# Kernel optimization log

Hardware: AMD Instinct MI355X
Metric: run time of the kernel (lower is better)

The kernel has to match this reference:

```python
import jax, jax.numpy as jnp
import numpy as np

NUM_HEADS = 8
NSCALE = 2  # len(sr_ratio) + 1 with sr_ratio=[2.0]


def setup_inputs() -> dict:
    key = jax.random.key(0)
    ks = jax.random.split(key, 12)
    B, Nq, Np, C, n_up, N_all = 16, 1024, 1024, 512, 2048, 4096
    s = C ** -0.5  # keep attention logits in a sane range
    return {
        "query": jax.random.normal(ks[0], (Nq, B, C), jnp.float32),
        "key": jax.random.normal(ks[1], (Np, B, C), jnp.float32),
        "key_pos": jax.random.uniform(ks[2], (B, Np, 3), jnp.float32),
        "xyz_all": jax.random.uniform(ks[3], (B, N_all, 3), jnp.float32),
        "xyz_upsample": jax.random.uniform(ks[4], (B, n_up, 3), jnp.float32),
        "Wq": jax.random.normal(ks[5], (C, C), jnp.float32) * s,
        "Wkv1": jax.random.normal(ks[6], (C, C), jnp.float32) * s,
        "Wkv2": jax.random.normal(ks[7], (C, C), jnp.float32) * s,
        "fp_w": jax.random.normal(ks[8], (C, C), jnp.float32) * s,
        "fp_b": jnp.zeros((C,), jnp.float32),
        "proj_w": jax.random.normal(ks[9], (C, C), jnp.float32) * s,
        "proj_b": jnp.zeros((C,), jnp.float32),
    }


def _fp_upsample(xyz_up, key_pos, key_feats, fp_w, fp_b):
    """PointnetFPModuleUpSample: 3-NN inverse-distance feature interpolation
    from Np known points (key_pos) onto n_up target points, followed by a
    pointwise MLP (1x1 conv, BN folded) + ReLU.
    key_feats: (Np, B, C) -> returns (B, n_up, C)."""
    d2 = jnp.sum((xyz_up[:, :, None, :] - key_pos[:, None, :, :]) ** 2, axis=-1)  # (B, n, Np)
    negd, idx = jax.lax.top_k(-d2, 3)  # 3 nearest neighbors, (B, n, 3)
    w = 1.0 / (-negd + 1e-8)
    w = w / jnp.sum(w, axis=-1, keepdims=True)
    feats = jnp.transpose(key_feats, (1, 0, 2))  # (B, Np, C)
    g = jnp.take_along_axis(feats[:, None, :, :], idx[..., None], axis=2)  # (B, n, 3, C)
    interp = jnp.sum(g * w[..., None], axis=2)  # (B, n, C)
    return jax.nn.relu(interp @ fp_w.T + fp_b)


def reference(query, key, key_pos, xyz_all, xyz_upsample,
              Wq, Wkv1, Wkv2, fp_w, fp_b, proj_w, proj_b):
    Np, B, C = key.shape
    Nq = query.shape[0]
    H = NUM_HEADS
    nh = H // NSCALE  # heads per scale group
    hd = C // H
    scale = hd ** -0.5

    # NOTE: torch reshapes (N,B,C) -> (B,N,...) WITHOUT permuting first; we
    # replicate the identical row-major reshape for bit-faithful structure.
    q = (query @ Wq.T).reshape(B, Nq, H, hd).transpose(0, 2, 1, 3)  # (B,H,Nq,hd)

    def attend(qs, kv):
        k, v = kv[0], kv[1]
        a = jax.nn.softmax(jnp.einsum('bhqd,bhkd->bhqk', qs, k) * scale, axis=-1)
        o = jnp.einsum('bhqk,bhkd->bhqd', a, v)
        return o.transpose(0, 2, 1, 3).reshape(B, Nq, nh * hd)

    # scale 1: full-resolution keys
    kv1 = (key @ Wkv1.T).reshape(B, -1, 2, nh, hd).transpose(2, 0, 3, 1, 4)
    x1 = attend(q[:, :nh], kv1)

    # scale 2: FP-upsampled keys (sr_ratio=2.0 -> 2*base_np points)
    key2 = _fp_upsample(xyz_upsample, key_pos, key, fp_w, fp_b)  # (B, n, C)
    key2_nbc = key2.transpose(1, 0, 2)  # (n, B, C), matches permute(2,0,1) of (B,C,n)
    kv2 = (key2_nbc @ Wkv2.T).reshape(B, -1, 2, nh, hd).transpose(2, 0, 3, 1, 4)
    x2 = attend(q[:, nh:], kv2)

    x = jnp.concatenate([x1, x2], axis=-1) @ proj_w.T + proj_b  # (B, Nq, C)
    return x.transpose(1, 0, 2)  # (Nq, B, C)
```

## Files before the change

kernel.cpp:

```cpp
#include <hip/hip_runtime.h>
#include <cstdint>
#include <cstddef>

#define CD   512
#define BDIM 16
#define NQ   1024
#define NP   1024
#define NUP  2048

typedef unsigned short u16;
typedef short short8 __attribute__((ext_vector_type(8)));
typedef float f32x4  __attribute__((ext_vector_type(4)));
typedef uint32_t u32x4 __attribute__((ext_vector_type(4)));

#define GLOAD16(g, l) __builtin_amdgcn_global_load_lds( \
    (const __attribute__((address_space(1))) void*)(g), \
    (__attribute__((address_space(3))) void*)(l), 16, 0, 0)

__device__ __forceinline__ u16 rne_bf16(float x) {
  uint32_t u = __float_as_uint(x);
  return (u16)((u + 0x7fffu + ((u >> 16) & 1u)) >> 16);
}
__device__ __forceinline__ float bf2f(u16 v) {
  return __uint_as_float(((uint32_t)v) << 16);
}

__global__ __launch_bounds__(256) void prep_kernel(
    const float* __restrict__ query, u16* __restrict__ Qa,
    const float* __restrict__ key, u16* __restrict__ Ka,
    const float* __restrict__ Wq, const float* __restrict__ Wkv1,
    const float* __restrict__ projw, const float* __restrict__ fpw,
    const float* __restrict__ wkv2, u16* __restrict__ Wq2,
    u16* __restrict__ Wkv12, u16* __restrict__ proj2,
    u16* __restrict__ fpwb, u16* __restrict__ wkv2b,
    const float* __restrict__ key_pos, const float* __restrict__ xyz_up,
    int* __restrict__ idx_out, float* __restrict__ w_out)
{
  const int bx = blockIdx.x;
  const int tid = threadIdx.x;
  if (bx < 8832) {
    const float* in; u16* out; float scl = 1.0f; long u;
    if (bx < 8192) {
      in = (bx < 4096) ? query : key;
      out = (bx < 4096) ? Qa : Ka;
      u = (long)(bx & 4095) * 256 + tid;
    } else {
      const int job = (bx - 8192) >> 7;
      in  = (job == 0) ? Wq  : (job == 1) ? Wkv1  : (job == 2) ? projw : (job == 3) ? fpw  : wkv2;
      out = (job == 0) ? Wq2 : (job == 1) ? Wkv12 : (job == 2) ? proj2 : (job == 3) ? fpwb : wkv2b;
      if (job == 0) scl = 0.18033688011112042f;
      u = (long)((bx - 8192) & 127) * 256 + tid;
    }
    const float* ip = in + u * 8;
    float v[8];
    *(float4*)&v[0] = *(const float4*)ip;
    *(float4*)&v[4] = *(const float4*)(ip + 4);
    short8 o;
#pragma unroll
    for (int i = 0; i < 8; ++i) o[i] = (short)rne_bf16(v[i] * scl);
    *(short8*)(out + u * 8) = o;
    return;
  }
  __shared__ __align__(16) float4 kp4[NP];
  const int kb = bx - 8832;
  const int b = kb >> 7;
  const int n0 = (kb & 127) * 16;
  const float* kpb = key_pos + (long)b * NP * 3;
#pragma unroll
  for (int s = 0; s < 4; ++s) {
    const int t = s * 256 + tid;
    kp4[t] = make_float4(kpb[t * 3], kpb[t * 3 + 1], kpb[t * 3 + 2], 0.0f);
  }
  __syncthreads();
  const int sc = tid & 15, pt = tid >> 4;
  const int n = n0 + pt;
  const float ux = xyz_up[(b * NUP + n) * 3 + 0];
  const float uy = xyz_up[(b * NUP + n) * 3 + 1];
  const float uz = xyz_up[(b * NUP + n) * 3 + 2];
  float e0 = 3.4e38f, e1 = 3.4e38f, e2 = 3.4e38f;
  int j0 = 0, j1 = 0, j2 = 0;
  for (int it = 0; it < 64; ++it) {
    const int j = it * 16 + sc;
    const float4 kv = kp4[j];
    const float dx = ux - kv.x, dy = uy - kv.y, dz = uz - kv.z;
    const float dd = dx * dx + dy * dy + dz * dz;
    if (dd < e2) {
      if (dd < e1) {
        e2 = e1; j2 = j1;
        if (dd < e0) { e1 = e0; j1 = j0; e0 = dd; j0 = j; }
        else         { e1 = dd; j1 = j; }
      } else { e2 = dd; j2 = j; }
    }
  }
#pragma unroll
  for (int ms = 1; ms <= 8; ms <<= 1) {
    const float pd0 = __shfl_xor(e0, ms), pd1 = __shfl_xor(e1, ms), pd2 = __shfl_xor(e2, ms);
    const int   pi0 = __shfl_xor(j0, ms), pi1 = __shfl_xor(j1, ms), pi2 = __shfl_xor(j2, ms);
    float cd[3] = {pd0, pd1, pd2};
    int   ci[3] = {pi0, pi1, pi2};
#pragma unroll
    for (int t = 0; t < 3; ++t) {
      const float dd = cd[t]; const int jj = ci[t];
      if (dd < e2 || (dd == e2 && jj < j2)) {
        if (dd < e1 || (dd == e1 && jj < j1)) {
          e2 = e1; j2 = j1;
          if (dd < e0 || (dd == e0 && jj < j0)) { e1 = e0; j1 = j0; e0 = dd; j0 = jj; }
          else                                  { e1 = dd; j1 = jj; }
        } else { e2 = dd; j2 = jj; }
      }
    }
  }
  if (sc == 0) {
    const float w0 = 1.0f / (e0 + 1e-8f);
    const float w1 = 1.0f / (e1 + 1e-8f);
    const float w2 = 1.0f / (e2 + 1e-8f);
    const float inv = 1.0f / ((w0 + w1) + w2);
    const long r = (long)b * NUP + n;
    idx_out[r * 3 + 0] = j0; idx_out[r * 3 + 1] = j1; idx_out[r * 3 + 2] = j2;
    w_out[r * 3 + 0] = w0 * inv; w_out[r * 3 + 1] = w1 * inv; w_out[r * 3 + 2] = w2 * inv;
  }
}

template<int AMODE, int OMODE, int KE, int NKT>
__device__ __forceinline__ void gemm_body64(
    u16* __restrict__ As, u16* __restrict__ Ws,
    const u16* __restrict__ A, const u16* __restrict__ W,
    const float* __restrict__ bias, void* __restrict__ outv,
    u16* __restrict__ Vt, const int m0, const int n0)
{
  const int tid = threadIdx.x;
  const int lane = tid & 63, wv = tid >> 6;
  const int rch = tid & 7;

  f32x4 acc[4][4];
#pragma unroll
  for (int mi = 0; mi < 4; ++mi)
#pragma unroll
    for (int ni = 0; ni < 4; ++ni)
#pragma unroll
      for (int r = 0; r < 4; ++r) acc[mi][ni][r] = 0.0f;

  const long rowb = (long)KE * 2;
  const char* gA[4]; const char* gW[4];
#pragma unroll
  for (int s = 0; s < 4; ++s) {
    const int row = s * 32 + (tid >> 3);
    const int gm = m0 + row;
    const long arow = (AMODE == 0) ? (long)gm : (long)(gm & 15) * 2048 + (gm >> 4);
    const int kb0 = (rch ^ (row & 7)) << 4;
    gA[s] = (const char*)A + arow * rowb + kb0;
    gW[s] = (const char*)W + (long)(n0 + row) * rowb + kb0;
  }
  const int wr = (wv >> 1) * 64, wc = (wv & 1) * 64;
  const int g = lane >> 4, cl = lane & 15;

  for (int kt = 0; kt < KE / 64; ++kt) {
#pragma unroll
    for (int s = 0; s < 4; ++s) {
      GLOAD16(gA[s], (char*)As + (s * 256 + tid) * 16);
      GLOAD16(gW[s], (char*)Ws + (s * 256 + tid) * 16);
      gA[s] += 128; gW[s] += 128;
    }
    __syncthreads();
#pragma unroll
    for (int kb = 0; kb < 2; ++kb) {
      short8 af[4], bf[4];
#pragma unroll
      for (int i = 0; i < 4; ++i) {
        const int ra = wr + i * 16 + cl;
        af[i] = *(const short8*)((const char*)As + ra * 128
                 + ((kb * 64 + g * 16) ^ ((ra & 7) << 4)));
        const int rb = wc + i * 16 + cl;
        bf[i] = *(const short8*)((const char*)Ws + rb * 128
                 + ((kb * 64 + g * 16) ^ ((rb & 7) << 4)));
      }
#pragma unroll
      for (int mi = 0; mi < 4; ++mi)
#pragma unroll
        for (int ni = 0; ni < 4; ++ni)
          acc[mi][ni] = __builtin_amdgcn_mfma_f32_16x16x32_bf16(af[mi], bf[ni], acc[mi][ni], 0, 0, 0);
    }
    __syncthreads();
  }

  if constexpr (OMODE == 3) {
    u16* T = As;
#pragma unroll
    for (int ni = 0; ni < 4; ++ni) {
      const int n = wc + ni * 16 + cl;
      const int swz = (n & 15) << 4;
      const int rb2 = n * 256;
#pragma unroll
      for (int mi = 0; mi < 4; ++mi) {
        uint32_t lo, hi;
        asm("v_cvt_pk_bf16_f32 %0, %1, %2" : "=v"(lo) : "v"(acc[mi][ni][0]), "v"(acc[mi][ni][1]));
        asm("v_cvt_pk_bf16_f32 %0, %1, %2" : "=v"(hi) : "v"(acc[mi][ni][2]), "v"(acc[mi][ni][3]));
        const int m2 = 2 * (wr + mi * 16 + g * 4);
        uint2 pk; pk.x = lo; pk.y = hi;
        *(uint2*)((char*)T + rb2 + (m2 ^ swz)) = pk;
      }
    }
    __syncthreads();
    const int nl = tid >> 1, mh = tid & 1;
    const int v = (n0 - 256) + nl;
    const int hh = v >> 6, dd = v & 63;
    const int bq = m0 / NKT;
    const int p0 = (m0 & (NKT - 1)) + mh * 64;
    u16* dst = Vt + ((size_t)((bq * 4 + hh) * 64 + dd)) * NKT + p0;
    const int swz = (nl & 15) << 4;
#pragma unroll
    for (int j = 0; j < 8; ++j) {
      const int m2 = mh * 128 + j * 16;
      const short8 val = *(const short8*)((const char*)T + nl * 256 + (m2 ^ swz));
      *(short8*)(dst + j * 8) = val;
    }
    return;
  } else {
#pragma unroll
    for (int mi = 0; mi < 4; ++mi)
#pragma unroll
      for (int ni = 0; ni < 4; ++ni)
#pragma unroll
        for (int r = 0; r < 4; ++r) {
          const int gm = m0 + wr + mi * 16 + g * 4 + r;
          const int gn = n0 + wc + ni * 16 + cl;
          float vv = acc[mi][ni][r];
          if (OMODE == 0) {
            ((u16*)outv)[(long)gm * 512 + gn] = rne_bf16(vv);
          } else if (OMODE == 1) {
            vv = fmaxf(vv + bias[gn], 0.0f);
            ((u16*)outv)[(long)gm * 512 + gn] = rne_bf16(vv);
          } else {
            vv += bias[gn];
            ((float*)outv)[((long)(gm & 1023) * BDIM + (gm >> 10)) * 512 + gn] = vv;
          }
        }
  }
}

template<int AMODE, int OMODE, int KE>
__global__ __launch_bounds__(256) void gemm_one(
    const u16* __restrict__ A, const u16* __restrict__ W,
    const float* __restrict__ bias, void* __restrict__ outv)
{
  __shared__ __align__(16) u16 SH[16384];
  gemm_body64<AMODE, OMODE, KE, 1024>(SH, SH + 8192, A, W, bias, outv, nullptr,
                                      blockIdx.x * 128, blockIdx.y * 128);
}

__global__ __launch_bounds__(256) void qkv1_interp_kernel(
    const u16* __restrict__ Qa, const u16* __restrict__ Wq2, u16* __restrict__ Qb,
    const u16* __restrict__ Ka, const u16* __restrict__ Wkv12,
    u16* __restrict__ KV1, u16* __restrict__ Vt1,
    const int* __restrict__ idx, const float* __restrict__ w, u16* __restrict__ IN2)
{
  __shared__ __align__(16) u16 SH[16384];
  const int bid = blockIdx.x;
  if (bid < 512) {
    gemm_body64<0, 0, 512, 1024>(SH, SH + 8192, Qa, Wq2, nullptr, Qb, nullptr,
                                 (bid >> 2) * 128, (bid & 3) * 128);
  } else if (bid < 1024) {
    const int t = bid - 512;
    const int n0 = (t & 3) * 128;
    if (n0 >= 256)
      gemm_body64<0, 3, 512, 1024>(SH, SH + 8192, Ka, Wkv12, nullptr, KV1, Vt1,
                                   (t >> 2) * 128, n0);
    else
      gemm_body64<0, 0, 512, 1024>(SH, SH + 8192, Ka, Wkv12, nullptr, KV1, nullptr,
                                   (t >> 2) * 128, n0);
  } else {
    const int t = threadIdx.x;
    const long r = (long)(bid - 1024) * 4 + (t >> 6);
    const int j = t & 63;
    const int b = (int)(r >> 11);
    const int j0 = idx[r * 3 + 0], j1 = idx[r * 3 + 1], j2 = idx[r * 3 + 2];
    const float w0 = w[r * 3 + 0], w1 = w[r * 3 + 1], w2 = w[r * 3 + 2];
    const short8 a0 = *(const short8*)(Ka + ((long)j0 * BDIM + b) * CD + j * 8);
    const short8 a1 = *(const short8*)(Ka + ((long)j1 * BDIM + b) * CD + j * 8);
    const short8 a2 = *(const short8*)(Ka + ((long)j2 * BDIM + b) * CD + j * 8);
    short8 o;
#pragma unroll
    for (int i = 0; i < 8; ++i)
      o[i] = (short)rne_bf16(bf2f((u16)a0[i]) * w0 + bf2f((u16)a1[i]) * w1
                           + bf2f((u16)a2[i]) * w2);
    *(short8*)(IN2 + r * CD + j * 8) = o;
  }
}

__global__ __launch_bounds__(256) void kv2_kernel(
    const u16* __restrict__ KEY2, const u16* __restrict__ wkv2b,
    u16* __restrict__ KV2, u16* __restrict__ Vt2)
{
  __shared__ __align__(16) u16 SH[16384];
  const int t = blockIdx.x;
  const int n0 = (t & 3) * 128;
  if (n0 >= 256)
    gemm_body64<1, 3, 512, 2048>(SH, SH + 8192, KEY2, wkv2b, nullptr, KV2, Vt2,
                                 (t >> 2) * 128, n0);
  else
    gemm_body64<1, 0, 512, 2048>(SH, SH + 8192, KEY2, wkv2b, nullptr, KV2, nullptr,
                                 (t >> 2) * 128, n0);
}

__global__ __launch_bounds__(256) void gemm_proj64_kernel(
    const u16* __restrict__ A, const u16* __restrict__ W,
    const float* __restrict__ bias, float* __restrict__ out)
{
  __shared__ __align__(16) u16 As[64 * 32];
  __shared__ __align__(16) u16 Ws[128 * 32];
  const int tid = threadIdx.x;
  const int lane = tid & 63, wv = tid >> 6;
  const int m0 = blockIdx.x * 64, n0 = blockIdx.y * 128;

  f32x4 acc[2][4];
#pragma unroll
  for (int mi = 0; mi < 2; ++mi)
#pragma unroll
    for (int ni = 0; ni < 4; ++ni)
#pragma unroll
      for (int r = 0; r < 4; ++r) acc[mi][ni][r] = 0.0f;

  const int ar = tid >> 2, ac = tid & 3;
  const char* gA = (const char*)A + (long)(m0 + ar) * 1024 + ((ac ^ (ar & 3)) << 4);
  const char* gW[2];
#pragma unroll
  for (int s = 0; s < 2; ++s) {
    const int rw = s * 64 + ar;
    gW[s] = (const char*)W + (long)(n0 + rw) * 1024 + ((ac ^ (rw & 3)) << 4);
  }
  const int wr = (wv >> 1) * 32, wc = (wv & 1) * 64;
  const int g = lane >> 4, cl = lane & 15;
  const int gx = (g ^ (cl & 3)) << 4;

  for (int kt = 0; kt < 16; ++kt) {
    GLOAD16(gA, (char*)As + tid * 16); gA += 64;
#pragma unroll
    for (int s = 0; s < 2; ++s) {
      GLOAD16(gW[s], (char*)Ws + (s * 256 + tid) * 16); gW[s] += 64;
    }
    __syncthreads();
    short8 af[2], bf[4];
#pragma unroll
    for (int i = 0; i < 2; ++i)
      af[i] = *(const short8*)((const char*)As + (wr + i * 16 + cl) * 64 + gx);
#pragma unroll
    for (int j = 0; j < 4; ++j)
      bf[j] = *(const short8*)((const char*)Ws + (wc + j * 16 + cl) * 64 + gx);
#pragma unroll
    for (int mi = 0; mi < 2; ++mi)
#pragma unroll
      for (int ni = 0; ni < 4; ++ni)
        acc[mi][ni] = __builtin_amdgcn_mfma_f32_16x16x32_bf16(af[mi], bf[ni], acc[mi][ni], 0, 0, 0);
    __syncthreads();
  }

#pragma unroll
  for (int mi = 0; mi < 2; ++mi)
#pragma unroll
    for (int ni = 0; ni < 4; ++ni)
#pragma unroll
      for (int r = 0; r < 4; ++r) {
        const int gm = m0 + wr + mi * 16 + g * 4 + r;
        const int gn = n0 + wc + ni * 16 + cl;
        out[((long)(gm & 1023) * BDIM + (gm >> 10)) * 512 + gn] = acc[mi][ni][r] + bias[gn];
      }
}

template<int NK>
__device__ __forceinline__ void attn_body(
    u16* __restrict__ Ks, u16* __restrict__ Vs,
    const u16* __restrict__ Q, const u16* __restrict__ KV,
    const u16* __restrict__ Vt, u16* __restrict__ X,
    const int h, const int sc, const int qt, const int b)
{
  const int tid = threadIdx.x;
  const int lane = tid & 63, wv = tid >> 6;
  const int g = lane >> 4, cl = lane & 15;

  const u16* qptr = Q + ((size_t)(b * 1024 + qt * 64 + wv * 16 + cl)) * 512
                      + (sc * 4 + h) * 64 + g * 8;
  const short8 qf0 = *(const short8*)qptr;
  const short8 qf1 = *(const short8*)(qptr + 32);

  f32x4 acc[4];
#pragma unroll
  for (int dj = 0; dj < 4; ++dj)
#pragma unroll
    for (int r = 0; r < 4; ++r) acc[dj][r] = 0.0f;
  float l = 0.0f;

  const char* kB = (const char*)(KV + (size_t)b * NK * 512 + h * 64);
  const char* vB = (const char*)(Vt + (size_t)((b * 4 + h) * 64) * NK);
  uint32_t koffL[4], voffL[4];
#pragma unroll
  for (int s = 0; s < 4; ++s) {
    const int c = s * 256 + tid;
    { const int rr = c >> 3, ch = c & 7;
      const int sig = (rr & 3) | ((rr >> 1) & 4);
      koffL[s] = rr * 1024 + ((ch ^ sig) << 4); }
    { const int rr = c >> 4, ch = c & 15;
      voffL[s] = rr * (NK * 2) + ((ch ^ (rr & 7)) << 4); }
  }

  int koffb[2][2];
#pragma unroll
  for (int half = 0; half < 2; ++half) {
    const int rest = ((cl & 12) << 1) + half * 4 + (cl & 3);
    const int swz = ((rest & 3) << 4) | ((rest & 8) << 3);
#pragma unroll
    for (int dh = 0; dh < 2; ++dh)
      koffb[half][dh] = rest * 128 + ((dh * 64 + g * 16) ^ swz);
  }
  int voffx[4][2];
#pragma unroll
  for (int dj = 0; dj < 4; ++dj) {
    const int vrow = dj * 16 + cl;
    const int base = vrow * 256 + ((g * 16) ^ ((vrow & 7) << 4));
    voffx[dj][0] = base; voffx[dj][1] = base ^ 64;
  }
  const int srcb = (lane & 48) | (g << 2);

  constexpr int NT = NK / 128;
#define ISSUE_K(kt_) { const char* kT_ = kB + (size_t)(kt_) * 131072; \
  _Pragma("unroll") for (int s_ = 0; s_ < 4; ++s_) \
    GLOAD16(kT_ + koffL[s_], (char*)Ks + s_ * 4096 + tid * 16); }
#define ISSUE_V(kt_) { const char* vT_ = vB + (size_t)(kt_) * 256; \
  _Pragma("unroll") for (int s_ = 0; s_ < 4; ++s_) \
    GLOAD16(vT_ + voffL[s_], (char*)Vs + s_ * 4096 + tid * 16); }

  asm volatile("s_waitcnt vmcnt(0)" ::: "memory");
  ISSUE_K(0);
  ISSUE_V(0);

  for (int kt = 0; kt < NT; ++kt) {
    asm volatile("s_waitcnt vmcnt(4)" ::: "memory");
    __builtin_amdgcn_s_barrier();
    __builtin_amdgcn_sched_barrier(0);

    f32x4 sv[8];
#pragma unroll
    for (int f = 0; f < 8; ++f)
#pragma unroll
      for (int r = 0; r < 4; ++r) sv[f][r] = 0.0f;
    __builtin_amdgcn_s_setprio(1);
#pragma unroll
    for (int ks = 0; ks < 4; ++ks)
#pragma unroll
      for (int half = 0; half < 2; ++half) {
        const int f = ks * 2 + half;
        const short8 ak0 = *(const short8*)((const char*)Ks + ks * 4096 + koffb[half][0]);
        const short8 ak1 = *(const short8*)((const char*)Ks + ks * 4096 + koffb[half][1]);
        sv[f] = __builtin_amdgcn_mfma_f32_16x16x32_bf16(ak0, qf0, sv[f], 0, 0, 0);
        sv[f] = __builtin_amdgcn_mfma_f32_16x16x32_bf16(ak1, qf1, sv[f], 0, 0, 0);
      }
    __builtin_amdgcn_s_setprio(0);

    asm volatile("s_waitcnt lgkmcnt(0)" ::: "memory");
    __builtin_amdgcn_s_barrier();
    __builtin_amdgcn_sched_barrier(0);
    if (kt + 1 < NT) { ISSUE_K(kt + 1); }

    float rs = 0.0f;
#pragma unroll
    for (int f = 0; f < 8; ++f)
#pragma unroll
      for (int r = 0; r < 4; ++r) {
        sv[f][r] = __builtin_amdgcn_exp2f(sv[f][r]);
        rs += sv[f][r];
      }
    rs += __shfl_xor(rs, 16);
    rs += __shfl_xor(rs, 32);
    l += rs;

    u32x4 pw[4];
#pragma unroll
    for (int ks = 0; ks < 4; ++ks) {
      asm("v_cvt_pk_bf16_f32 %0, %1, %2" : "=v"(pw[ks][0]) : "v"(sv[2*ks][0]),   "v"(sv[2*ks][1]));
      asm("v_cvt_pk_bf16_f32 %0, %1, %2" : "=v"(pw[ks][1]) : "v"(sv[2*ks][2]),   "v"(sv[2*ks][3]));
      asm("v_cvt_pk_bf16_f32 %0, %1, %2" : "=v"(pw[ks][2]) : "v"(sv[2*ks+1][0]), "v"(sv[2*ks+1][1]));
      asm("v_cvt_pk_bf16_f32 %0, %1, %2" : "=v"(pw[ks][3]) : "v"(sv[2*ks+1][2]), "v"(sv[2*ks+1][3]));
    }

    if (kt + 1 < NT) { asm volatile("s_waitcnt vmcnt(4)" ::: "memory"); }
    else             { asm volatile("s_waitcnt vmcnt(0)" ::: "memory"); }
    __builtin_amdgcn_s_barrier();
    __builtin_amdgcn_sched_barrier(0);

    __builtin_amdgcn_s_setprio(1);
#pragma unroll
    for (int ks = 0; ks < 4; ++ks) {
      const short8 pa = __builtin_bit_cast(short8, pw[ks]);
#pragma unroll
      for (int dj = 0; dj < 4; ++dj) {
        const short8 bv = *(const short8*)((const char*)Vs +
                          ((ks >> 1) * 128 + voffx[dj][ks & 1]));
        acc[dj] = __builtin_amdgcn_mfma_f32_16x16x32_bf16(pa, bv, acc[dj], 0, 0, 0);
      }
    }
    __builtin_amdgcn_s_setprio(0);

    asm volatile("s_waitcnt lgkmcnt(0)" ::: "memory");
    __builtin_amdgcn_s_barrier();
    __builtin_amdgcn_sched_barrier(0);
    if (kt + 1 < NT) { ISSUE_V(kt + 1); }
  }
#undef ISSUE_K
#undef ISSUE_V

  const float inv = 1.0f / l;
  float invr[4];
#pragma unroll
  for (int r = 0; r < 4; ++r) invr[r] = __shfl(inv, srcb | r);
#pragma unroll
  for (int dj = 0; dj < 4; ++dj)
#pragma unroll
    for (int r = 0; r < 4; ++r) {
      const long gq = b * 1024 + qt * 64 + wv * 16 + g * 4 + r;
      X[gq * 512 + sc * 256 + h * 64 + dj * 16 + cl] = rne_bf16(acc[dj][r] * invr[r]);
    }
}

__global__ __launch_bounds__(256, 4) void attn_fused_kernel(
    const u16* __restrict__ Q,
    const u16* __restrict__ KV1, const u16* __restrict__ KV2,
    const u16* __restrict__ Vt1, const u16* __restrict__ Vt2,
    u16* __restrict__ X)
{
  __shared__ __align__(16) u16 Ks[128 * 64];
  __shared__ __align__(16) u16 Vs[64 * 128];
  const int d = blockIdx.x + (blockIdx.y << 4) + (blockIdx.z << 8);
  const int qt = (d >> 3) & 15;
  const int grp = (d & 7) + ((d >> 7) << 3);
  const int b = grp & 15, z = grp >> 4;
  if (z < 4) attn_body<1024>(Ks, Vs, Q, KV1, Vt1, X, z, 0, qt, b);
  else       attn_body<2048>(Ks, Vs, Q, KV2, Vt2, X, z - 4, 1, qt, b);
}

extern "C" void kernel_launch(void* const* d_in, const int* in_sizes, int n_in,
                              void* d_out, int out_size, void* d_ws, size_t ws_size,
                              hipStream_t stream) {
  const float* query   = (const float*)d_in[0];
  const float* key     = (const float*)d_in[1];
  const float* key_pos = (const float*)d_in[2];
  const float* xyz_up  = (const float*)d_in[4];
  const float* Wq      = (const float*)d_in[5];
  const float* Wkv1    = (const float*)d_in[6];
  const float* Wkv2    = (const float*)d_in[7];
  const float* fp_w    = (const float*)d_in[8];
  const float* fp_b    = (const float*)d_in[9];
  const float* proj_w  = (const float*)d_in[10];
  const float* proj_b  = (const float*)d_in[11];

  char* ws = (char*)d_ws;
  const size_t MB = 1024 * 1024;
  u16*  Qa    = (u16*)(ws + 0);
  u16*  Ka    = (u16*)(ws + 16 * MB);
  u16*  Qb    = (u16*)(ws + 32 * MB);
  u16*  KV1   = (u16*)(ws + 48 * MB);
  u16*  IN2   = (u16*)(ws + 64 * MB);
  u16*  KEY2  = (u16*)(ws + 96 * MB);
  u16*  Vt1   = (u16*)(ws + 128 * MB);
  u16*  Vt2   = (u16*)(ws + 136 * MB);
  u16*  Wq2   = (u16*)(ws + 152 * MB);
  u16*  Wkv12 = (u16*)(ws + 152 * MB + 512 * 1024);
  u16*  proj2 = (u16*)(ws + 153 * MB);
  u16*  fpwb  = (u16*)(ws + 153 * MB + 512 * 1024);
  u16*  wkv2b = (u16*)(ws + 154 * MB);
  int*  idxb  = (int*)(ws + 155 * MB);
  float* wb   = (float*)(ws + 156 * MB);
  u16*  KV2   = IN2;
  u16*  X     = Qa;

  prep_kernel<<<dim3(10880), 256, 0, stream>>>(
      query, Qa, key, Ka, Wq, Wkv1, proj_w, fp_w, Wkv2,
      Wq2, Wkv12, proj2, fpwb, wkv2b, key_pos, xyz_up, idxb, wb);
  qkv1_interp_kernel<<<dim3(9216), 256, 0, stream>>>(
      Qa, Wq2, Qb, Ka, Wkv12, KV1, Vt1, idxb, wb, IN2);
  gemm_one<0, 1, 512><<<dim3(256, 4), 256, 0, stream>>>(IN2, fpwb, fp_b, KEY2);
  kv2_kernel<<<dim3(1024), 256, 0, stream>>>(KEY2, wkv2b, KV2, Vt2);
  attn_fused_kernel<<<dim3(16, 16, 8), 256, 0, stream>>>(Qb, KV1, KV2, Vt1, Vt2, X);
  gemm_proj64_kernel<<<dim3(256, 4), 256, 0, stream>>>(X, proj2, proj_b, (float*)d_out);
}
```

Baseline: 234.3 us.

## Co-schedule scale-1 attention with KV2 GEMM in a single launch

The fused attention kernel is split. Scale-1 attention blocks, which depend only on Q and KV1, now run in the same grid as the KV2 projection GEMM. A separate kernel then handles scale-2 attention after KV2 is ready. This overlaps independent work and fills the GPU better during the GEMM. The cost is a heterogeneous kernel with GEMM-sized shared memory and no occupancy hint for the attention blocks, plus tail imbalance between the two block types.

```diff
diff --git a/kernel.cpp b/kernel.cpp
--- a/kernel.cpp
+++ b/kernel.cpp
@@ -246,6 +246,160 @@
   __shared__ __align__(16) u16 SH[16384];
   gemm_body64<AMODE, OMODE, KE, 1024>(SH, SH + 8192, A, W, bias, outv, nullptr,
                                       blockIdx.x * 128, blockIdx.y * 128);
+}
+
+template<int NK>
+__device__ __forceinline__ void attn_body(
+    u16* __restrict__ Ks, u16* __restrict__ Vs,
+    const u16* __restrict__ Q, const u16* __restrict__ KV,
+    const u16* __restrict__ Vt, u16* __restrict__ X,
+    const int h, const int sc, const int qt, const int b)
+{
+  const int tid = threadIdx.x;
+  const int lane = tid & 63, wv = tid >> 6;
+  const int g = lane >> 4, cl = lane & 15;
+
+  const u16* qptr = Q + ((size_t)(b * 1024 + qt * 64 + wv * 16 + cl)) * 512
+                      + (sc * 4 + h) * 64 + g * 8;
+  const short8 qf0 = *(const short8*)qptr;
+  const short8 qf1 = *(const short8*)(qptr + 32);
+
+  f32x4 acc[4];
+#pragma unroll
+  for (int dj = 0; dj < 4; ++dj)
+#pragma unroll
+    for (int r = 0; r < 4; ++r) acc[dj][r] = 0.0f;
+  float l = 0.0f;
+
+  const char* kB = (const char*)(KV + (size_t)b * NK * 512 + h * 64);
+  const char* vB = (const char*)(Vt + (size_t)((b * 4 + h) * 64) * NK);
+  uint32_t koffL[4], voffL[4];
+#pragma unroll
+  for (int s = 0; s < 4; ++s) {
+    const int c = s * 256 + tid;
+    { const int rr = c >> 3, ch = c & 7;
+      const int sig = (rr & 3) | ((rr >> 1) & 4);
+      koffL[s] = rr * 1024 + ((ch ^ sig) << 4); }
+    { const int rr = c >> 4, ch = c & 15;
+      voffL[s] = rr * (NK * 2) + ((ch ^ (rr & 7)) << 4); }
+  }
+
+  int koffb[2][2];
+#pragma unroll
+  for (int half = 0; half < 2; ++half) {
+    const int rest = ((cl & 12) << 1) + half * 4 + (cl & 3);
+    const int swz = ((rest & 3) << 4) | ((rest & 8) << 3);
+#pragma unroll
+    for (int dh = 0; dh < 2; ++dh)
+      koffb[half][dh] = rest * 128 + ((dh * 64 + g * 16) ^ swz);
+  }
+  int voffx[4][2];
+#pragma unroll
+  for (int dj = 0; dj < 4; ++dj) {
+    const int vrow = dj * 16 + cl;
+    const int base = vrow * 256 + ((g * 16) ^ ((vrow & 7) << 4));
+    voffx[dj][0] = base; voffx[dj][1] = base ^ 64;
+  }
+  const int srcb = (lane & 48) | (g << 2);
+
+  constexpr int NT = NK / 128;
+#define ISSUE_K(kt_) { const char* kT_ = kB + (size_t)(kt_) * 131072; \
+  _Pragma("unroll") for (int s_ = 0; s_ < 4; ++s_) \
+    GLOAD16(kT_ + koffL[s_], (char*)Ks + s_ * 4096 + tid * 16); }
+#define ISSUE_V(kt_) { const char* vT_ = vB + (size_t)(kt_) * 256; \
+  _Pragma("unroll") for (int s_ = 0; s_ < 4; ++s_) \
+    GLOAD16(vT_ + voffL[s_], (char*)Vs + s_ * 4096 + tid * 16); }
+
+  asm volatile("s_waitcnt vmcnt(0)" ::: "memory");
+  ISSUE_K(0);
+  ISSUE_V(0);
+
+  for (int kt = 0; kt < NT; ++kt) {
+    asm volatile("s_waitcnt vmcnt(4)" ::: "memory");
+    __builtin_amdgcn_s_barrier();
+    __builtin_amdgcn_sched_barrier(0);
+
+    f32x4 sv[8];
+#pragma unroll
+    for (int f = 0; f < 8; ++f)
+#pragma unroll
+      for (int r = 0; r < 4; ++r) sv[f][r] = 0.0f;
+    __builtin_amdgcn_s_setprio(1);
+#pragma unroll
+    for (int ks = 0; ks < 4; ++ks)
+#pragma unroll
+      for (int half = 0; half < 2; ++half) {
+        const int f = ks * 2 + half;
+        const short8 ak0 = *(const short8*)((const char*)Ks + ks * 4096 + koffb[half][0]);
+        const short8 ak1 = *(const short8*)((const char*)Ks + ks * 4096 + koffb[half][1]);
+        sv[f] = __builtin_amdgcn_mfma_f32_16x16x32_bf16(ak0, qf0, sv[f], 0, 0, 0);
+        sv[f] = __builtin_amdgcn_mfma_f32_16x16x32_bf16(ak1, qf1, sv[f], 0, 0, 0);
+      }
+    __builtin_amdgcn_s_setprio(0);
+
+    asm volatile("s_waitcnt lgkmcnt(0)" ::: "memory");
+    __builtin_amdgcn_s_barrier();
+    __builtin_amdgcn_sched_barrier(0);
+    if (kt + 1 < NT) { ISSUE_K(kt + 1); }
+
+    float rs = 0.0f;
+#pragma unroll
+    for (int f = 0; f < 8; ++f)
+#pragma unroll
+      for (int r = 0; r < 4; ++r) {
+        sv[f][r] = __builtin_amdgcn_exp2f(sv[f][r]);
+        rs += sv[f][r];
+      }
+    rs += __shfl_xor(rs, 16);
+    rs += __shfl_xor(rs, 32);
+    l += rs;
+
+    u32x4 pw[4];
+#pragma unroll
+    for (int ks = 0; ks < 4; ++ks) {
+      asm("v_cvt_pk_bf16_f32 %0, %1, %2" : "=v"(pw[ks][0]) : "v"(sv[2*ks][0]),   "v"(sv[2*ks][1]));
+      asm("v_cvt_pk_bf16_f32 %0, %1, %2" : "=v"(pw[ks][1]) : "v"(sv[2*ks][2]),   "v"(sv[2*ks][3]));
+      asm("v_cvt_pk_bf16_f32 %0, %1, %2" : "=v"(pw[ks][2]) : "v"(sv[2*ks+1][0]), "v"(sv[2*ks+1][1]));
+      asm("v_cvt_pk_bf16_f32 %0, %1, %2" : "=v"(pw[ks][3]) : "v"(sv[2*ks+1][2]), "v"(sv[2*ks+1][3]));
+    }
+
+    if (kt + 1 < NT) { asm volatile("s_waitcnt vmcnt(4)" ::: "memory"); }
+    else             { asm volatile("s_waitcnt vmcnt(0)" ::: "memory"); }
+    __builtin_amdgcn_s_barrier();
+    __builtin_amdgcn_sched_barrier(0);
+
+    __builtin_amdgcn_s_setprio(1);
+#pragma unroll
+    for (int ks = 0; ks < 4; ++ks) {
+      const short8 pa = __builtin_bit_cast(short8, pw[ks]);
+#pragma unroll
+      for (int dj = 0; dj < 4; ++dj) {
+        const short8 bv = *(const short8*)((const char*)Vs +
+                          ((ks >> 1) * 128 + voffx[dj][ks & 1]));
+        acc[dj] = __builtin_amdgcn_mfma_f32_16x16x32_bf16(pa, bv, acc[dj], 0, 0, 0);
+      }
+    }
+    __builtin_amdgcn_s_setprio(0);
+
+    asm volatile("s_waitcnt lgkmcnt(0)" ::: "memory");
+    __builtin_amdgcn_s_barrier();
+    __builtin_amdgcn_sched_barrier(0);
+    if (kt + 1 < NT) { ISSUE_V(kt + 1); }
+  }
+#undef ISSUE_K
+#undef ISSUE_V
+
+  const float inv = 1.0f / l;
+  float invr[4];
+#pragma unroll
+  for (int r = 0; r < 4; ++r) invr[r] = __shfl(inv, srcb | r);
+#pragma unroll
+  for (int dj = 0; dj < 4; ++dj)
+#pragma unroll
+    for (int r = 0; r < 4; ++r) {
+      const long gq = b * 1024 + qt * 64 + wv * 16 + g * 4 + r;
+      X[gq * 512 + sc * 256 + h * 64 + dj * 16 + cl] = rne_bf16(acc[dj][r] * invr[r]);
+    }
 }
 
 __global__ __launch_bounds__(256) void qkv1_interp_kernel(
@@ -287,19 +441,42 @@
   }
 }
 
-__global__ __launch_bounds__(256) void kv2_kernel(
+__global__ __launch_bounds__(256) void kv2_attn1_kernel(
     const u16* __restrict__ KEY2, const u16* __restrict__ wkv2b,
-    u16* __restrict__ KV2, u16* __restrict__ Vt2)
+    u16* __restrict__ KV2, u16* __restrict__ Vt2,
+    const u16* __restrict__ Qb, const u16* __restrict__ KV1,
+    const u16* __restrict__ Vt1, u16* __restrict__ X)
 {
   __shared__ __align__(16) u16 SH[16384];
-  const int t = blockIdx.x;
-  const int n0 = (t & 3) * 128;
-  if (n0 >= 256)
-    gemm_body64<1, 3, 512, 2048>(SH, SH + 8192, KEY2, wkv2b, nullptr, KV2, Vt2,
-                                 (t >> 2) * 128, n0);
-  else
-    gemm_body64<1, 0, 512, 2048>(SH, SH + 8192, KEY2, wkv2b, nullptr, KV2, nullptr,
-                                 (t >> 2) * 128, n0);
+  const int bid = blockIdx.x;
+  if (bid < 1024) {
+    const int n0 = (bid & 3) * 128;
+    if (n0 >= 256)
+      gemm_body64<1, 3, 512, 2048>(SH, SH + 8192, KEY2, wkv2b, nullptr, KV2, Vt2,
+                                   (bid >> 2) * 128, n0);
+    else
+      gemm_body64<1, 0, 512, 2048>(SH, SH + 8192, KEY2, wkv2b, nullptr, KV2, nullptr,
+                                   (bid >> 2) * 128, n0);
+  } else {
+    const int d = bid - 1024;
+    const int qt = (d >> 3) & 15;
+    const int grp = (d & 7) + ((d >> 7) << 3);
+    const int b = grp & 15, h = grp >> 4;
+    attn_body<1024>(SH, SH + 8192, Qb, KV1, Vt1, X, h, 0, qt, b);
+  }
+}
+
+__global__ __launch_bounds__(256, 4) void attn_s2_kernel(
+    const u16* __restrict__ Q, const u16* __restrict__ KV2,
+    const u16* __restrict__ Vt2, u16* __restrict__ X)
+{
+  __shared__ __align__(16) u16 Ks[128 * 64];
+  __shared__ __align__(16) u16 Vs[64 * 128];
+  const int d = blockIdx.x + (blockIdx.y << 4) + (blockIdx.z << 8);
+  const int qt = (d >> 3) & 15;
+  const int grp = (d & 7) + ((d >> 7) << 3);
+  const int b = grp & 15, h = grp >> 4;
+  attn_body<2048>(Ks, Vs, Q, KV2, Vt2, X, h, 1, qt, b);
 }
 
 __global__ __launch_bounds__(256) void gemm_proj64_kernel(
@@ -364,176 +541,6 @@
         const int gn = n0 + wc + ni * 16 + cl;
         out[((long)(gm & 1023) * BDIM + (gm >> 10)) * 512 + gn] = acc[mi][ni][r] + bias[gn];
       }
-}
-
-template<int NK>
-__device__ __forceinline__ void attn_body(
-    u16* __restrict__ Ks, u16* __restrict__ Vs,
-    const u16* __restrict__ Q, const u16* __restrict__ KV,
-    const u16* __restrict__ Vt, u16* __restrict__ X,
-    const int h, const int sc, const int qt, const int b)
-{
-  const int tid = threadIdx.x;
-  const int lane = tid & 63, wv = tid >> 6;
-  const int g = lane >> 4, cl = lane & 15;
-
-  const u16* qptr = Q + ((size_t)(b * 1024 + qt * 64 + wv * 16 + cl)) * 512
-                      + (sc * 4 + h) * 64 + g * 8;
-  const short8 qf0 = *(const short8*)qptr;
-  const short8 qf1 = *(const short8*)(qptr + 32);
-
-  f32x4 acc[4];
-#pragma unroll
-  for (int dj = 0; dj < 4; ++dj)
-#pragma unroll
-    for (int r = 0; r < 4; ++r) acc[dj][r] = 0.0f;
-  float l = 0.0f;
-
-  const char* kB = (const char*)(KV + (size_t)b * NK * 512 + h * 64);
-  const char* vB = (const char*)(Vt + (size_t)((b * 4 + h) * 64) * NK);
-  uint32_t koffL[4], voffL[4];
-#pragma unroll
-  for (int s = 0; s < 4; ++s) {
-    const int c = s * 256 + tid;
-    { const int rr = c >> 3, ch = c & 7;
-      const int sig = (rr & 3) | ((rr >> 1) & 4);
-      koffL[s] = rr * 1024 + ((ch ^ sig) << 4); }
-    { const int rr = c >> 4, ch = c & 15;
-      voffL[s] = rr * (NK * 2) + ((ch ^ (rr & 7)) << 4); }
-  }
-
-  int koffb[2][2];
-#pragma unroll
-  for (int half = 0; half < 2; ++half) {
-    const int rest = ((cl & 12) << 1) + half * 4 + (cl & 3);
-    const int swz = ((rest & 3) << 4) | ((rest & 8) << 3);
-#pragma unroll
-    for (int dh = 0; dh < 2; ++dh)
-      koffb[half][dh] = rest * 128 + ((dh * 64 + g * 16) ^ swz);
-  }
-  int voffx[4][2];
-#pragma unroll
-  for (int dj = 0; dj < 4; ++dj) {
-    const int vrow = dj * 16 + cl;
-    const int base = vrow * 256 + ((g * 16) ^ ((vrow & 7) << 4));
-    voffx[dj][0] = base; voffx[dj][1] = base ^ 64;
-  }
-  const int srcb = (lane & 48) | (g << 2);
-
-  constexpr int NT = NK / 128;
-#define ISSUE_K(kt_) { const char* kT_ = kB + (size_t)(kt_) * 131072; \
-  _Pragma("unroll") for (int s_ = 0; s_ < 4; ++s_) \
-    GLOAD16(kT_ + koffL[s_], (char*)Ks + s_ * 4096 + tid * 16); }
-#define ISSUE_V(kt_) { const char* vT_ = vB + (size_t)(kt_) * 256; \
-  _Pragma("unroll") for (int s_ = 0; s_ < 4; ++s_) \
-    GLOAD16(vT_ + voffL[s_], (char*)Vs + s_ * 4096 + tid * 16); }
-
-  asm volatile("s_waitcnt vmcnt(0)" ::: "memory");
-  ISSUE_K(0);
-  ISSUE_V(0);
-
-  for (int kt = 0; kt < NT; ++kt) {
-    asm volatile("s_waitcnt vmcnt(4)" ::: "memory");
-    __builtin_amdgcn_s_barrier();
-    __builtin_amdgcn_sched_barrier(0);
-
-    f32x4 sv[8];
-#pragma unroll
-    for (int f = 0; f < 8; ++f)
-#pragma unroll
-      for (int r = 0; r < 4; ++r) sv[f][r] = 0.0f;
-    __builtin_amdgcn_s_setprio(1);
-#pragma unroll
-    for (int ks = 0; ks < 4; ++ks)
-#pragma unroll
-      for (int half = 0; half < 2; ++half) {
-        const int f = ks * 2 + half;
-        const short8 ak0 = *(const short8*)((const char*)Ks + ks * 4096 + koffb[half][0]);
-        const short8 ak1 = *(const short8*)((const char*)Ks + ks * 4096 + koffb[half][1]);
-        sv[f] = __builtin_amdgcn_mfma_f32_16x16x32_bf16(ak0, qf0, sv[f], 0, 0, 0);
-        sv[f] = __builtin_amdgcn_mfma_f32_16x16x32_bf16(ak1, qf1, sv[f], 0, 0, 0);
-      }
-    __builtin_amdgcn_s_setprio(0);
-
-    asm volatile("s_waitcnt lgkmcnt(0)" ::: "memory");
-    __builtin_amdgcn_s_barrier();
-    __builtin_amdgcn_sched_barrier(0);
-    if (kt + 1 < NT) { ISSUE_K(kt + 1); }
-
-    float rs = 0.0f;
-#pragma unroll
-    for (int f = 0; f < 8; ++f)
-#pragma unroll
-      for (int r = 0; r < 4; ++r) {
-        sv[f][r] = __builtin_amdgcn_exp2f(sv[f][r]);
-        rs += sv[f][r];
-      }
-    rs += __shfl_xor(rs, 16);
-    rs += __shfl_xor(rs, 32);
-    l += rs;
-
-    u32x4 pw[4];
-#pragma unroll
-    for (int ks = 0; ks < 4; ++ks) {
-      asm("v_cvt_pk_bf16_f32 %0, %1, %2" : "=v"(pw[ks][0]) : "v"(sv[2*ks][0]),   "v"(sv[2*ks][1]));
-      asm("v_cvt_pk_bf16_f32 %0, %1, %2" : "=v"(pw[ks][1]) : "v"(sv[2*ks][2]),   "v"(sv[2*ks][3]));
-      asm("v_cvt_pk_bf16_f32 %0, %1, %2" : "=v"(pw[ks][2]) : "v"(sv[2*ks+1][0]), "v"(sv[2*ks+1][1]));
-      asm("v_cvt_pk_bf16_f32 %0, %1, %2" : "=v"(pw[ks][3]) : "v"(sv[2*ks+1][2]), "v"(sv[2*ks+1][3]));
-    }
-
-    if (kt + 1 < NT) { asm volatile("s_waitcnt vmcnt(4)" ::: "memory"); }
-    else             { asm volatile("s_waitcnt vmcnt(0)" ::: "memory"); }
-    __builtin_amdgcn_s_barrier();
-    __builtin_amdgcn_sched_barrier(0);
-
-    __builtin_amdgcn_s_setprio(1);
-#pragma unroll
-    for (int ks = 0; ks < 4; ++ks) {
-      const short8 pa = __builtin_bit_cast(short8, pw[ks]);
-#pragma unroll
-      for (int dj = 0; dj < 4; ++dj) {
-        const short8 bv = *(const short8*)((const char*)Vs +
-                          ((ks >> 1) * 128 + voffx[dj][ks & 1]));
-        acc[dj] = __builtin_amdgcn_mfma_f32_16x16x32_bf16(pa, bv, acc[dj], 0, 0, 0);
-      }
-    }
-    __builtin_amdgcn_s_setprio(0);
-
-    asm volatile("s_waitcnt lgkmcnt(0)" ::: "memory");
-    __builtin_amdgcn_s_barrier();
-    __builtin_amdgcn_sched_barrier(0);
-    if (kt + 1 < NT) { ISSUE_V(kt + 1); }
-  }
-#undef ISSUE_K
-#undef ISSUE_V
-
-  const float inv = 1.0f / l;
-  float invr[4];
-#pragma unroll
-  for (int r = 0; r < 4; ++r) invr[r] = __shfl(inv, srcb | r);
-#pragma unroll
-  for (int dj = 0; dj < 4; ++dj)
-#pragma unroll
-    for (int r = 0; r < 4; ++r) {
-      const long gq = b * 1024 + qt * 64 + wv * 16 + g * 4 + r;
-      X[gq * 512 + sc * 256 + h * 64 + dj * 16 + cl] = rne_bf16(acc[dj][r] * invr[r]);
-    }
-}
-
-__global__ __launch_bounds__(256, 4) void attn_fused_kernel(
-    const u16* __restrict__ Q,
-    const u16* __restrict__ KV1, const u16* __restrict__ KV2,
-    const u16* __restrict__ Vt1, const u16* __restrict__ Vt2,
-    u16* __restrict__ X)
-{
-  __shared__ __align__(16) u16 Ks[128 * 64];
-  __shared__ __align__(16) u16 Vs[64 * 128];
-  const int d = blockIdx.x + (blockIdx.y << 4) + (blockIdx.z << 8);
-  const int qt = (d >> 3) & 15;
-  const int grp = (d & 7) + ((d >> 7) << 3);
-  const int b = grp & 15, z = grp >> 4;
-  if (z < 4) attn_body<1024>(Ks, Vs, Q, KV1, Vt1, X, z, 0, qt, b);
-  else       attn_body<2048>(Ks, Vs, Q, KV2, Vt2, X, z - 4, 1, qt, b);
 }
 
 extern "C" void kernel_launch(void* const* d_in, const int* in_sizes, int n_in,
@@ -577,7 +584,8 @@
   qkv1_interp_kernel<<<dim3(9216), 256, 0, stream>>>(
       Qa, Wq2, Qb, Ka, Wkv12, KV1, Vt1, idxb, wb, IN2);
   gemm_one<0, 1, 512><<<dim3(256, 4), 256, 0, stream>>>(IN2, fpwb, fp_b, KEY2);
-  kv2_kernel<<<dim3(1024), 256, 0, stream>>>(KEY2, wkv2b, KV2, Vt2);
-  attn_fused_kernel<<<dim3(16, 16, 8), 256, 0, stream>>>(Qb, KV1, KV2, Vt1, Vt2, X);
+  kv2_attn1_kernel<<<dim3(2048), 256, 0, stream>>>(
+      KEY2, wkv2b, KV2, Vt2, Qb, KV1, Vt1, X);
+  attn_s2_kernel<<<dim3(16, 16, 4), 256, 0, stream>>>(Qb, KV2, Vt2, X);
   gemm_proj64_kernel<<<dim3(256, 4), 256, 0, stream>>>(X, proj2, proj_b, (float*)d_out);
 }
```

Result: no change. 237.8 us (+1.5%).

## Switch attention to 32x32x16 MFMA with 128-query tiles and merged K/V loads

Applied to the files above, without the earlier changes.

Rewrites the fused attention body to use 32x32x16 bf16 MFMA instead of 16x16x32, so each wave handles 32 queries and each block 128. That halves the grid and doubles K/V reuse per LDS tile. K and V tiles are now loaded together, with a full vmcnt(0) wait, instead of being staged separately, and the LDS swizzles are redone for the new fragment layout. The softmax row sum no longer needs per-tile shuffles, but the merged loads lose the previous overlap of V loading with QK compute and fewer blocks run concurrently.

```diff
diff --git a/kernel.cpp b/kernel.cpp
--- a/kernel.cpp
+++ b/kernel.cpp
@@ -11,6 +11,7 @@
 typedef unsigned short u16;
 typedef short short8 __attribute__((ext_vector_type(8)));
 typedef float f32x4  __attribute__((ext_vector_type(4)));
+typedef float f32x16 __attribute__((ext_vector_type(16)));
 typedef uint32_t u32x4 __attribute__((ext_vector_type(4)));
 
 #define GLOAD16(g, l) __builtin_amdgcn_global_load_lds( \
@@ -367,7 +368,7 @@
 }
 
 template<int NK>
-__device__ __forceinline__ void attn_body(
+__device__ __forceinline__ void attn_body32(
     u16* __restrict__ Ks, u16* __restrict__ Vs,
     const u16* __restrict__ Q, const u16* __restrict__ KV,
     const u16* __restrict__ Vt, u16* __restrict__ X,
@@ -375,18 +376,17 @@
 {
   const int tid = threadIdx.x;
   const int lane = tid & 63, wv = tid >> 6;
-  const int g = lane >> 4, cl = lane & 15;
-
-  const u16* qptr = Q + ((size_t)(b * 1024 + qt * 64 + wv * 16 + cl)) * 512
-                      + (sc * 4 + h) * 64 + g * 8;
-  const short8 qf0 = *(const short8*)qptr;
-  const short8 qf1 = *(const short8*)(qptr + 32);
-
-  f32x4 acc[4];
-#pragma unroll
-  for (int dj = 0; dj < 4; ++dj)
-#pragma unroll
-    for (int r = 0; r < 4; ++r) acc[dj][r] = 0.0f;
+  const int hi = lane >> 5, ql = lane & 31;
+
+  const u16* qptr = Q + ((size_t)(b * 1024 + qt * 128 + wv * 32 + ql)) * 512
+                      + (sc * 4 + h) * 64 + hi * 8;
+  short8 qf[4];
+#pragma unroll
+  for (int t = 0; t < 4; ++t) qf[t] = *(const short8*)(qptr + t * 16);
+
+  f32x16 acc0, acc1;
+#pragma unroll
+  for (int i = 0; i < 16; ++i) { acc0[i] = 0.0f; acc1[i] = 0.0f; }
   float l = 0.0f;
 
   const char* kB = (const char*)(KV + (size_t)b * NK * 512 + h * 64);
@@ -395,132 +395,94 @@
 #pragma unroll
   for (int s = 0; s < 4; ++s) {
     const int c = s * 256 + tid;
-    { const int rr = c >> 3, ch = c & 7;
-      const int sig = (rr & 3) | ((rr >> 1) & 4);
-      koffL[s] = rr * 1024 + ((ch ^ sig) << 4); }
-    { const int rr = c >> 4, ch = c & 15;
-      voffL[s] = rr * (NK * 2) + ((ch ^ (rr & 7)) << 4); }
-  }
-
-  int koffb[2][2];
-#pragma unroll
-  for (int half = 0; half < 2; ++half) {
-    const int rest = ((cl & 12) << 1) + half * 4 + (cl & 3);
-    const int swz = ((rest & 3) << 4) | ((rest & 8) << 3);
-#pragma unroll
-    for (int dh = 0; dh < 2; ++dh)
-      koffb[half][dh] = rest * 128 + ((dh * 64 + g * 16) ^ swz);
-  }
-  int voffx[4][2];
-#pragma unroll
-  for (int dj = 0; dj < 4; ++dj) {
-    const int vrow = dj * 16 + cl;
-    const int base = vrow * 256 + ((g * 16) ^ ((vrow & 7) << 4));
-    voffx[dj][0] = base; voffx[dj][1] = base ^ 64;
-  }
-  const int srcb = (lane & 48) | (g << 2);
+    { const int key = c >> 3, cp = c & 7;
+      koffL[s] = key * 1024 + ((cp ^ (key & 7)) << 4); }
+    { const int d = c >> 4, cp = c & 15;
+      voffL[s] = d * (NK * 2) + ((cp ^ (d & 15)) << 4); }
+  }
+
+  const int sel = ((ql >> 2) ^ (ql >> 3)) & 1;
+  const int kpi = ql ^ (sel ? 12 : 0);
+  int kaddr[4];
+#pragma unroll
+  for (int t = 0; t < 4; ++t)
+    kaddr[t] = kpi * 128 + (((t * 2 + hi) ^ (kpi & 7)) << 4);
+  const int vx = ql & 15;
 
   constexpr int NT = NK / 128;
-#define ISSUE_K(kt_) { const char* kT_ = kB + (size_t)(kt_) * 131072; \
-  _Pragma("unroll") for (int s_ = 0; s_ < 4; ++s_) \
-    GLOAD16(kT_ + koffL[s_], (char*)Ks + s_ * 4096 + tid * 16); }
-#define ISSUE_V(kt_) { const char* vT_ = vB + (size_t)(kt_) * 256; \
-  _Pragma("unroll") for (int s_ = 0; s_ < 4; ++s_) \
-    GLOAD16(vT_ + voffL[s_], (char*)Vs + s_ * 4096 + tid * 16); }
-
-  asm volatile("s_waitcnt vmcnt(0)" ::: "memory");
-  ISSUE_K(0);
-  ISSUE_V(0);
+#define ISSUE_KV(kt_) { \
+  const char* kT_ = kB + (size_t)(kt_) * 131072; \
+  const char* vT_ = vB + (size_t)(kt_) * 256; \
+  _Pragma("unroll") for (int s_ = 0; s_ < 4; ++s_) { \
+    GLOAD16(kT_ + koffL[s_], (char*)Ks + (s_ * 256 + tid) * 16); \
+    GLOAD16(vT_ + voffL[s_], (char*)Vs + (s_ * 256 + tid) * 16); } }
+
+  ISSUE_KV(0);
 
   for (int kt = 0; kt < NT; ++kt) {
-    asm volatile("s_waitcnt vmcnt(4)" ::: "memory");
+    asm volatile("s_waitcnt vmcnt(0)" ::: "memory");
     __builtin_amdgcn_s_barrier();
     __builtin_amdgcn_sched_barrier(0);
 
-    f32x4 sv[8];
-#pragma unroll
-    for (int f = 0; f < 8; ++f)
-#pragma unroll
-      for (int r = 0; r < 4; ++r) sv[f][r] = 0.0f;
-    __builtin_amdgcn_s_setprio(1);
-#pragma unroll
-    for (int ks = 0; ks < 4; ++ks)
-#pragma unroll
-      for (int half = 0; half < 2; ++half) {
-        const int f = ks * 2 + half;
-        const short8 ak0 = *(const short8*)((const char*)Ks + ks * 4096 + koffb[half][0]);
-        const short8 ak1 = *(const short8*)((const char*)Ks + ks * 4096 + koffb[half][1]);
-        sv[f] = __builtin_amdgcn_mfma_f32_16x16x32_bf16(ak0, qf0, sv[f], 0, 0, 0);
-        sv[f] = __builtin_amdgcn_mfma_f32_16x16x32_bf16(ak1, qf1, sv[f], 0, 0, 0);
-      }
-    __builtin_amdgcn_s_setprio(0);
+#pragma unroll
+    for (int blk = 0; blk < 4; ++blk) {
+      f32x16 sv;
+#pragma unroll
+      for (int i = 0; i < 16; ++i) sv[i] = 0.0f;
+      __builtin_amdgcn_s_setprio(1);
+#pragma unroll
+      for (int t = 0; t < 4; ++t) {
+        const short8 kf = *(const short8*)((const char*)Ks + blk * 4096 + kaddr[t]);
+        sv = __builtin_amdgcn_mfma_f32_32x32x16_bf16(kf, qf[t], sv, 0, 0, 0);
+      }
+      __builtin_amdgcn_s_setprio(0);
+#pragma unroll
+      for (int i = 0; i < 16; ++i) {
+        sv[i] = __builtin_amdgcn_exp2f(sv[i]);
+        l += sv[i];
+      }
+#pragma unroll
+      for (int sh = 0; sh < 2; ++sh) {
+        u32x4 pw;
+        asm("v_cvt_pk_bf16_f32 %0, %1, %2" : "=v"(pw[0]) : "v"(sv[8*sh+0]), "v"(sv[8*sh+1]));
+        asm("v_cvt_pk_bf16_f32 %0, %1, %2" : "=v"(pw[1]) : "v"(sv[8*sh+2]), "v"(sv[8*sh+3]));
+        asm("v_cvt_pk_bf16_f32 %0, %1, %2" : "=v"(pw[2]) : "v"(sv[8*sh+4]), "v"(sv[8*sh+5]));
+        asm("v_cvt_pk_bf16_f32 %0, %1, %2" : "=v"(pw[3]) : "v"(sv[8*sh+6]), "v"(sv[8*sh+7]));
+        const short8 pa = __builtin_bit_cast(short8, pw);
+        const int step = blk * 2 + sh;
+        const int vchunk = ((step * 2 + hi) ^ vx) << 4;
+        __builtin_amdgcn_s_setprio(1);
+        {
+          const short8 vf0 = *(const short8*)((const char*)Vs + ql * 256 + vchunk);
+          acc0 = __builtin_amdgcn_mfma_f32_32x32x16_bf16(pa, vf0, acc0, 0, 0, 0);
+          const short8 vf1 = *(const short8*)((const char*)Vs + (32 + ql) * 256 + vchunk);
+          acc1 = __builtin_amdgcn_mfma_f32_32x32x16_bf16(pa, vf1, acc1, 0, 0, 0);
+        }
+        __builtin_amdgcn_s_setprio(0);
+      }
+    }
 
     asm volatile("s_waitcnt lgkmcnt(0)" ::: "memory");
+    __builtin_amdgcn_sched_barrier(0);
     __builtin_amdgcn_s_barrier();
-    __builtin_amdgcn_sched_barrier(0);
-    if (kt + 1 < NT) { ISSUE_K(kt + 1); }
-
-    float rs = 0.0f;
-#pragma unroll
-    for (int f = 0; f < 8; ++f)
-#pragma unroll
-      for (int r = 0; r < 4; ++r) {
-        sv[f][r] = __builtin_amdgcn_exp2f(sv[f][r]);
-        rs += sv[f][r];
-      }
-    rs += __shfl_xor(rs, 16);
-    rs += __shfl_xor(rs, 32);
-    l += rs;
-
-    u32x4 pw[4];
-#pragma unroll
-    for (int ks = 0; ks < 4; ++ks) {
-      asm("v_cvt_pk_bf16_f32 %0, %1, %2" : "=v"(pw[ks][0]) : "v"(sv[2*ks][0]),   "v"(sv[2*ks][1]));
-      asm("v_cvt_pk_bf16_f32 %0, %1, %2" : "=v"(pw[ks][1]) : "v"(sv[2*ks][2]),   "v"(sv[2*ks][3]));
-      asm("v_cvt_pk_bf16_f32 %0, %1, %2" : "=v"(pw[ks][2]) : "v"(sv[2*ks+1][0]), "v"(sv[2*ks+1][1]));
-      asm("v_cvt_pk_bf16_f32 %0, %1, %2" : "=v"(pw[ks][3]) : "v"(sv[2*ks+1][2]), "v"(sv[2*ks+1][3]));
-    }
-
-    if (kt + 1 < NT) { asm volatile("s_waitcnt vmcnt(4)" ::: "memory"); }
-    else             { asm volatile("s_waitcnt vmcnt(0)" ::: "memory"); }
-    __builtin_amdgcn_s_barrier();
-    __builtin_amdgcn_sched_barrier(0);
-
-    __builtin_amdgcn_s_setprio(1);
-#pragma unroll
-    for (int ks = 0; ks < 4; ++ks) {
-      const short8 pa = __builtin_bit_cast(short8, pw[ks]);
-#pragma unroll
-      for (int dj = 0; dj < 4; ++dj) {
-        const short8 bv = *(const short8*)((const char*)Vs +
-                          ((ks >> 1) * 128 + voffx[dj][ks & 1]));
-        acc[dj] = __builtin_amdgcn_mfma_f32_16x16x32_bf16(pa, bv, acc[dj], 0, 0, 0);
-      }
-    }
-    __builtin_amdgcn_s_setprio(0);
-
-    asm volatile("s_waitcnt lgkmcnt(0)" ::: "memory");
-    __builtin_amdgcn_s_barrier();
-    __builtin_amdgcn_sched_barrier(0);
-    if (kt + 1 < NT) { ISSUE_V(kt + 1); }
-  }
-#undef ISSUE_K
-#undef ISSUE_V
-
+    if (kt + 1 < NT) { ISSUE_KV(kt + 1); }
+  }
+#undef ISSUE_KV
+
+  l += __shfl_xor(l, 32);
   const float inv = 1.0f / l;
-  float invr[4];
-#pragma unroll
-  for (int r = 0; r < 4; ++r) invr[r] = __shfl(inv, srcb | r);
-#pragma unroll
-  for (int dj = 0; dj < 4; ++dj)
-#pragma unroll
-    for (int r = 0; r < 4; ++r) {
-      const long gq = b * 1024 + qt * 64 + wv * 16 + g * 4 + r;
-      X[gq * 512 + sc * 256 + h * 64 + dj * 16 + cl] = rne_bf16(acc[dj][r] * invr[r]);
-    }
-}
-
-__global__ __launch_bounds__(256, 4) void attn_fused_kernel(
+  const long qbase = (long)b * 1024 + qt * 128 + wv * 32;
+#pragma unroll
+  for (int i = 0; i < 16; ++i) {
+    const int row = (i & 3) + 8 * (i >> 2) + 4 * hi;
+    const float ir = __shfl(inv, row);
+    const long go = (qbase + row) * 512 + sc * 256 + h * 64 + ql;
+    X[go]      = rne_bf16(acc0[i] * ir);
+    X[go + 32] = rne_bf16(acc1[i] * ir);
+  }
+}
+
+__global__ __launch_bounds__(256, 4) void attn_fused32_kernel(
     const u16* __restrict__ Q,
     const u16* __restrict__ KV1, const u16* __restrict__ KV2,
     const u16* __restrict__ Vt1, const u16* __restrict__ Vt2,
@@ -528,12 +490,12 @@
 {
   __shared__ __align__(16) u16 Ks[128 * 64];
   __shared__ __align__(16) u16 Vs[64 * 128];
-  const int d = blockIdx.x + (blockIdx.y << 4) + (blockIdx.z << 8);
-  const int qt = (d >> 3) & 15;
-  const int grp = (d & 7) + ((d >> 7) << 3);
+  const int d = blockIdx.x;
+  const int qt = (d >> 3) & 7;
+  const int grp = (d & 7) | ((d >> 6) << 3);
   const int b = grp & 15, z = grp >> 4;
-  if (z < 4) attn_body<1024>(Ks, Vs, Q, KV1, Vt1, X, z, 0, qt, b);
-  else       attn_body<2048>(Ks, Vs, Q, KV2, Vt2, X, z - 4, 1, qt, b);
+  if (z < 4) attn_body32<1024>(Ks, Vs, Q, KV1, Vt1, X, z, 0, qt, b);
+  else       attn_body32<2048>(Ks, Vs, Q, KV2, Vt2, X, z - 4, 1, qt, b);
 }
 
 extern "C" void kernel_launch(void* const* d_in, const int* in_sizes, int n_in,
@@ -578,6 +540,6 @@
       Qa, Wq2, Qb, Ka, Wkv12, KV1, Vt1, idxb, wb, IN2);
   gemm_one<0, 1, 512><<<dim3(256, 4), 256, 0, stream>>>(IN2, fpwb, fp_b, KEY2);
   kv2_kernel<<<dim3(1024), 256, 0, stream>>>(KEY2, wkv2b, KV2, Vt2);
-  attn_fused_kernel<<<dim3(16, 16, 8), 256, 0, stream>>>(Qb, KV1, KV2, Vt1, Vt2, X);
+  attn_fused32_kernel<<<dim3(1024), 256, 0, stream>>>(Qb, KV1, KV2, Vt1, Vt2, X);
   gemm_proj64_kernel<<<dim3(256, 4), 256, 0, stream>>>(X, proj2, proj_b, (float*)d_out);
 }
```

New measurement: 236.9 us. Within noise of the previous version (+1.1%).
